# Optimization experiments

Hardware: AMD Instinct MI355X
Metric: run time of the kernel (lower is better)

## Reference

```python
import jax, jax.numpy as jnp
import numpy as np
from jax import lax

NUM_GROUPS = 16
POOL_KS = 2
CLAMP_MIN = 0.0
CLAMP_MAX = 1.0
EPS = 1e-5


def setup_inputs() -> dict:
    key = jax.random.key(0)
    k1, k2, k3, k4, k5 = jax.random.split(key, 5)
    B, Cin, H, W = 32, 64, 128, 128
    Cout, K = 128, 3
    x = jax.random.normal(k1, (B, Cin, H, W), dtype=jnp.float32)
    fan_in = Cin * K * K
    bound = 1.0 / np.sqrt(fan_in)
    conv_w = jax.random.uniform(k2, (Cout, Cin, K, K), jnp.float32, -bound, bound)
    conv_b = jax.random.uniform(k3, (Cout,), jnp.float32, -bound, bound)
    gn_w = jnp.ones((Cout,), jnp.float32)
    gn_b = jnp.zeros((Cout,), jnp.float32)
    scale = jnp.ones((Cout, 1, 1), jnp.float32)
    return {"x": x, "conv_w": conv_w, "conv_b": conv_b,
            "gn_w": gn_w, "gn_b": gn_b, "scale": scale}


def reference(x, conv_w, conv_b, gn_w, gn_b, scale):
    # Conv2d, stride=1, padding=0  -> (B, Cout, Ho, Wo)
    y = lax.conv_general_dilated(
        x, conv_w, window_strides=(1, 1), padding="VALID",
        dimension_numbers=("NCHW", "OIHW", "NCHW"))
    y = y + conv_b[None, :, None, None]
    B, C, H, W = y.shape
    G = NUM_GROUPS
    # GroupNorm (biased variance, as in torch)
    yg = y.reshape(B, G, C // G, H, W)
    mean = jnp.mean(yg, axis=(2, 3, 4), keepdims=True)
    var = jnp.mean(jnp.square(yg), axis=(2, 3, 4), keepdims=True) - jnp.square(mean)
    yn = (yg - mean) * lax.rsqrt(var + EPS)
    yn = yn.reshape(B, C, H, W) * gn_w[None, :, None, None] + gn_b[None, :, None, None]
    # per-channel scale
    yn = yn * scale[None, :, :, :]
    # MaxPool2d(kernel=POOL_KS, stride=POOL_KS), VALID
    pooled = lax.reduce_window(
        yn, -jnp.inf, lax.max,
        window_dimensions=(1, 1, POOL_KS, POOL_KS),
        window_strides=(1, 1, POOL_KS, POOL_KS),
        padding="VALID")
    return jnp.clip(pooled, CLAMP_MIN, CLAMP_MAX)
```

## Files before the change

kernel.cpp:

```cpp
#include <hip/hip_runtime.h>
#include <stdint.h>
#include <stddef.h>

#define HIN 128
#define WIN 128
#define CINC 64
#define COUTC 128
#define HO 126
#define WO 126
#define HP 63
#define WP 63
#define NB 32
#define NG 16

typedef __bf16 bf16x8 __attribute__((ext_vector_type(8)));
typedef float f32x16 __attribute__((ext_vector_type(16)));

#define AS1U(p) ((const __attribute__((address_space(1))) unsigned int*)(p))
#define AS3U(p) ((__attribute__((address_space(3))) unsigned int*)(p))

#define WAITVM_(n) asm volatile("s_waitcnt vmcnt(" #n ")" ::: "memory")
#define WAITVM(n) WAITVM_(n)

__device__ __forceinline__ unsigned int f2bf(float f) {
  unsigned int u = __float_as_uint(f);
  return (u + 0x7fffu + ((u >> 16) & 1u)) >> 16;
}

__global__ __launch_bounds__(256) void wtrans_k(const float* __restrict__ w,
                                                unsigned short* __restrict__ wt2,
                                                float* __restrict__ stats) {
  int i = blockIdx.x * 256 + threadIdx.x;
  if (i < 1024) stats[i] = 0.0f;
  if (i >= 73728) return;
  int j = i & 7;
  int co = (i >> 3) & 127;
  int th = i >> 10;
  int half = th & 1, ks = (th >> 1) & 3, tap = th >> 3;
  int kh = tap / 3, kw = tap - 3 * kh;
  int cin = ks * 16 + half * 8 + j;
  float v = w[((co * CINC + cin) * 3 + kh) * 3 + kw];
  wt2[i] = (unsigned short)f2bf(v);
}

__global__ __launch_bounds__(256, 3) void conv_k(const float* __restrict__ x,
                                                 const unsigned short* __restrict__ wt2,
                                                 const float* __restrict__ conv_b,
                                                 float* __restrict__ out,
                                                 float* __restrict__ stats) {
  __shared__ __align__(16) unsigned int x_lds[10 * 18 * 32];
  __shared__ __align__(16) unsigned int w_lds[4096];

  int t = threadIdx.x;
  int lane = t & 63, wave = t >> 6;
  int wh = wave >> 1, wc = wave & 1;
  int tw = blockIdx.x & 7, th = blockIdx.x >> 3;
  int b = blockIdx.y;
  int oh0 = th * 8, ow0 = tw * 16;
  int half = lane >> 5, m = lane & 31;
  int rot4 = (((int)blockIdx.x + b) % 9) * 4;
  const unsigned int* wg = (const unsigned int*)wt2;
  int wdma_src = wave * 256 + lane * 4;
  int wdma_dst = wave * 256;

#pragma unroll
  for (int j = 0; j < 2; ++j) {
    int rs = j + rot4;
    if (rs >= 36) rs -= 36;
    __builtin_amdgcn_global_load_lds(AS1U(wg + rs * 1024 + wdma_src),
                                     AS3U(&w_lds[j * 1024 + wdma_dst]), 16, 0, 0);
  }

  float bias[2];
#pragma unroll
  for (int nt = 0; nt < 2; ++nt) bias[nt] = conv_b[wc * 64 + nt * 32 + m];

  const float* xb = x + (size_t)b * CINC * HIN * WIN;
#pragma unroll
  for (int k = 0; k < 7; ++k) {
    int i = k * 256 + t;
    if (i < 1600) {
      int c4 = i % 5;
      int j = i / 5;
      int p = j & 31;
      int r = j >> 5;
      int gr = oh0 + r;
      int gc0 = ow0 + c4 * 4;
      float4 v0 = make_float4(0.f, 0.f, 0.f, 0.f);
      float4 v1 = v0;
      if (gr < HIN && gc0 < WIN) {
        const float* base = xb + ((size_t)(2 * p) * HIN + gr) * WIN + gc0;
        v0 = *(const float4*)base;
        v1 = *(const float4*)(base + HIN * WIN);
      }
      float e0[4] = {v0.x, v0.y, v0.z, v0.w};
      float e1[4] = {v1.x, v1.y, v1.z, v1.w};
#pragma unroll
      for (int cc = 0; cc < 4; ++cc) {
        int c = c4 * 4 + cc;
        if (c < 18) {
          unsigned int d = f2bf(e0[cc]) | (f2bf(e1[cc]) << 16);
          x_lds[(r * 18 + c) * 32 + (p ^ ((c & 7) << 2))] = d;
        }
      }
    }
  }
  __syncthreads();

  f32x16 acc[2][2];
#pragma unroll
  for (int nt = 0; nt < 2; ++nt)
#pragma unroll
    for (int mt = 0; mt < 2; ++mt)
#pragma unroll
      for (int r = 0; r < 16; ++r) acc[mt][nt][r] = bias[nt];

  int prb = wh * 4 + (m >> 4);
  int pcc = m & 15;
  int h4 = half * 4;
  int wbl = half * 512 + wc * 256 + m * 4;

#define CONV_KS(ks_, VM, DO_DMA)                                               \
  {                                                                            \
    if (DO_DMA) {                                                              \
      int rs2 = rsb + (ks_) + 2;                                               \
      if (rs2 >= 36) rs2 -= 36;                                                \
      __builtin_amdgcn_global_load_lds(                                        \
          AS1U(wg + rs2 * 1024 + wdma_src),                                    \
          AS3U(&w_lds[(((ks_) + 2) & 3) * 1024 + wdma_dst]), 16, 0, 0);        \
    }                                                                          \
    WAITVM(VM);                                                                \
    __builtin_amdgcn_s_barrier();                                              \
    __builtin_amdgcn_sched_barrier(0);                                         \
    int ax = ((ks_)*8 + h4) ^ swz;                                             \
    bf16x8 afr0 = __builtin_bit_cast(bf16x8, *(const uint4*)&x_lds[ra0 + ax]); \
    bf16x8 afr1 = __builtin_bit_cast(bf16x8, *(const uint4*)&x_lds[ra1 + ax]); \
    int wb = (ks_)*1024 + wbl;                                                 \
    bf16x8 bfr0 = __builtin_bit_cast(bf16x8, *(const uint4*)&w_lds[wb]);       \
    bf16x8 bfr1 = __builtin_bit_cast(bf16x8, *(const uint4*)&w_lds[wb + 128]); \
    __builtin_amdgcn_s_setprio(1);                                             \
    acc[0][0] = __builtin_amdgcn_mfma_f32_32x32x16_bf16(afr0, bfr0, acc[0][0], 0, 0, 0); \
    acc[1][0] = __builtin_amdgcn_mfma_f32_32x32x16_bf16(afr1, bfr0, acc[1][0], 0, 0, 0); \
    acc[0][1] = __builtin_amdgcn_mfma_f32_32x32x16_bf16(afr0, bfr1, acc[0][1], 0, 0, 0); \
    acc[1][1] = __builtin_amdgcn_mfma_f32_32x32x16_bf16(afr1, bfr1, acc[1][1], 0, 0, 0); \
    __builtin_amdgcn_s_setprio(0);                                             \
  }

#pragma unroll 1
  for (int tp = 0; tp < 8; ++tp) {
    int rsb = tp * 4 + rot4;
    if (rsb >= 36) rsb -= 36;
    int tap = rsb >> 2;
    int kh = (tap * 11) >> 5;
    int kw = tap - 3 * kh;
    int c = pcc + kw;
    int swz = (c & 7) << 2;
    int ra0 = (prb + kh) * 576 + c * 32;
    int ra1 = ra0 + 2 * 576;
    CONV_KS(0, 2, 1)
    CONV_KS(1, 2, 1)
    CONV_KS(2, 2, 1)
    CONV_KS(3, 2, 1)
  }
  {
    int rsb = 32 + rot4;
    if (rsb >= 36) rsb -= 36;
    int tap = rsb >> 2;
    int kh = (tap * 11) >> 5;
    int kw = tap - 3 * kh;
    int c = pcc + kw;
    int swz = (c & 7) << 2;
    int ra0 = (prb + kh) * 576 + c * 32;
    int ra1 = ra0 + 2 * 576;
    CONV_KS(0, 2, 1)
    CONV_KS(1, 2, 1)
    CONV_KS(2, 1, 0)
    CONV_KS(3, 0, 0)
  }
#undef CONV_KS

  float s[2] = {0.f, 0.f}, qs[2] = {0.f, 0.f};
#pragma unroll
  for (int nt = 0; nt < 2; ++nt) {
#pragma unroll
    for (int mt = 0; mt < 2; ++mt) {
#pragma unroll
      for (int reg = 0; reg < 16; ++reg) {
        int c16 = (reg & 3) + 4 * half + 8 * ((reg >> 2) & 1);
        int r8 = wh * 4 + mt * 2 + (reg >> 3);
        if ((oh0 + r8) < HO && (ow0 + c16) < WO) {
          float v = acc[mt][nt][reg];
          s[nt] += v;
          qs[nt] += v * v;
        }
      }
    }
  }
#pragma unroll
  for (int nt = 0; nt < 2; ++nt) {
    float sv = s[nt], qv = qs[nt];
    sv += __shfl_xor(sv, 32);
    qv += __shfl_xor(qv, 32);
    sv += __shfl_down(sv, 4, 8);
    qv += __shfl_down(qv, 4, 8);
    sv += __shfl_down(sv, 2, 8);
    qv += __shfl_down(qv, 2, 8);
    sv += __shfl_down(sv, 1, 8);
    qv += __shfl_down(qv, 1, 8);
    if (half == 0 && (m & 7) == 0) {
      int g = wc * 8 + nt * 4 + (m >> 3);
      atomicAdd(&stats[(b * NG + g) * 2 + 0], sv);
      atomicAdd(&stats[(b * NG + g) * 2 + 1], qv);
    }
  }

  __syncthreads();

#pragma unroll
  for (int nt = 0; nt < 2; ++nt) {
    int co = wc * 64 + nt * 32 + m;
#pragma unroll
    for (int mt = 0; mt < 2; ++mt) {
      int oh2l = wh * 2 + mt;
#pragma unroll
      for (int i = 0; i < 4; ++i) {
        int r0 = 2 * i;
        int ow2l = (i & 1) + 2 * half + 4 * (i >> 1);
        float mx = fmaxf(fmaxf(acc[mt][nt][r0], acc[mt][nt][r0 + 1]),
                         fmaxf(acc[mt][nt][r0 + 8], acc[mt][nt][r0 + 9]));
        x_lds[co * 34 + oh2l * 8 + ow2l] = __float_as_uint(mx);
      }
    }
  }
  __syncthreads();

#pragma unroll
  for (int i = 0; i < 2; ++i) {
    int row = t * 2 + i;
    int co = row >> 2, oh2l = row & 3;
    int oh2 = th * 4 + oh2l;
    if (oh2 < HP) {
      const uint2* src = (const uint2*)&x_lds[co * 34 + oh2l * 8];
      uint2 d0 = src[0], d1 = src[1], d2 = src[2], d3 = src[3];
      unsigned int v[8] = {d0.x, d0.y, d1.x, d1.y, d2.x, d2.y, d3.x, d3.y};
      float* ob = out + ((size_t)(b * COUTC + co) * HP + oh2) * WP + tw * 8;
      int n = (tw == 7) ? 7 : 8;
#pragma unroll
      for (int e = 0; e < 8; ++e)
        if (e < n) ob[e] = __uint_as_float(v[e]);
    }
  }
}

__global__ __launch_bounds__(256) void fin_k(float* __restrict__ out,
                                             const float* __restrict__ stats,
                                             const float* __restrict__ gn_w,
                                             const float* __restrict__ gn_b,
                                             const float* __restrict__ scale) {
  const int plane = HP * WP;
  const float inv_cnt = 1.0f / (8.0f * HO * WO);
  int bc = blockIdx.x;
  int c = bc & 127, b = bc >> 7;
  int g = c >> 3;
  float su = stats[(b * NG + g) * 2 + 0];
  float sq = stats[(b * NG + g) * 2 + 1];
  float mean = su * inv_cnt;
  float var = fmaxf(sq * inv_cnt - mean * mean, 0.f);
  float rstd = rsqrtf(var + 1e-5f);
  float gw = gn_w[c], sc = scale[c];
  float A = rstd * gw * sc;
  float Bo = (gn_b[c] - mean * rstd * gw) * sc;

  float* p = out + (size_t)bc * plane;
  int t = threadIdx.x;
  int head = (4 - (bc & 3)) & 3;
  if (t < head) p[t] = fminf(fmaxf(fmaf(p[t], A, Bo), 0.0f), 1.0f);
  int n4 = (plane - head) >> 2;
  float4* p4 = (float4*)(p + head);
  for (int i = t; i < n4; i += 256) {
    float4 v = p4[i];
    v.x = fminf(fmaxf(fmaf(v.x, A, Bo), 0.0f), 1.0f);
    v.y = fminf(fmaxf(fmaf(v.y, A, Bo), 0.0f), 1.0f);
    v.z = fminf(fmaxf(fmaf(v.z, A, Bo), 0.0f), 1.0f);
    v.w = fminf(fmaxf(fmaf(v.w, A, Bo), 0.0f), 1.0f);
    p4[i] = v;
  }
  int done = head + (n4 << 2);
  int tail = plane - done;
  if (t < tail) p[done + t] = fminf(fmaxf(fmaf(p[done + t], A, Bo), 0.0f), 1.0f);
}

extern "C" void kernel_launch(void* const* d_in, const int* in_sizes, int n_in,
                              void* d_out, int out_size, void* d_ws, size_t ws_size,
                              hipStream_t stream) {
  const float* x      = (const float*)d_in[0];
  const float* conv_w = (const float*)d_in[1];
  const float* conv_b = (const float*)d_in[2];
  const float* gn_w   = (const float*)d_in[3];
  const float* gn_b   = (const float*)d_in[4];
  const float* scale  = (const float*)d_in[5];
  float* out = (float*)d_out;

  float* stats        = (float*)d_ws;
  unsigned short* wt2 = (unsigned short*)((char*)d_ws + 4096);

  wtrans_k<<<288, 256, 0, stream>>>(conv_w, wt2, stats);

  conv_k<<<dim3(128, NB), 256, 0, stream>>>(x, wt2, conv_b, out, stats);

  fin_k<<<4096, 256, 0, stream>>>(out, stats, gn_w, gn_b, scale);
}
```

Before: 366.3 us.

## Give each wave a private weight ring buffer and drop per-step block barriers

Each wave now DMAs its own copy of the weight slices it needs into a private 3-slot LDS ring, instead of the four waves cooperatively loading one shared 4-slot buffer. Because no wave reads another wave's DMA output, the s_barrier before every k-step is removed and only a per-wave vmcnt wait remains. The cost is more LDS (weights duplicated across waves, 24 KB vs 16 KB) and twice the global-to-LDS DMA traffic for weights. This may reduce occupancy under the 3-blocks-per-CU launch bound.

Result: slower. 381.3 us (+4.1%).

```diff
diff --git a/kernel.cpp b/kernel.cpp
--- a/kernel.cpp
+++ b/kernel.cpp
@@ -49,7 +49,7 @@
                                                  float* __restrict__ out,
                                                  float* __restrict__ stats) {
   __shared__ __align__(16) unsigned int x_lds[10 * 18 * 32];
-  __shared__ __align__(16) unsigned int w_lds[4096];
+  __shared__ __align__(16) unsigned int w_lds[6144];
 
   int t = threadIdx.x;
   int lane = t & 63, wave = t >> 6;
@@ -60,15 +60,17 @@
   int half = lane >> 5, m = lane & 31;
   int rot4 = (((int)blockIdx.x + b) % 9) * 4;
   const unsigned int* wg = (const unsigned int*)wt2;
-  int wdma_src = wave * 256 + lane * 4;
-  int wdma_dst = wave * 256;
+  int wsrc0 = wc * 256 + lane * 4;
+  int wring = wave * 1536;
 
 #pragma unroll
   for (int j = 0; j < 2; ++j) {
     int rs = j + rot4;
     if (rs >= 36) rs -= 36;
-    __builtin_amdgcn_global_load_lds(AS1U(wg + rs * 1024 + wdma_src),
-                                     AS3U(&w_lds[j * 1024 + wdma_dst]), 16, 0, 0);
+    const unsigned int* s0 = wg + rs * 1024 + wsrc0;
+    __builtin_amdgcn_global_load_lds(AS1U(s0), AS3U(&w_lds[wring + j * 512]), 16, 0, 0);
+    __builtin_amdgcn_global_load_lds(AS1U(s0 + 512),
+                                     AS3U(&w_lds[wring + j * 512 + 256]), 16, 0, 0);
   }
 
   float bias[2];
@@ -118,24 +120,26 @@
   int prb = wh * 4 + (m >> 4);
   int pcc = m & 15;
   int h4 = half * 4;
-  int wbl = half * 512 + wc * 256 + m * 4;
-
-#define CONV_KS(ks_, VM, DO_DMA)                                               \
+  int hm = half * 256 + m * 4;
+
+#define CONV_KS(ks_, VM, DO_DMA, SLOT, DSLOT)                                  \
   {                                                                            \
     if (DO_DMA) {                                                              \
       int rs2 = rsb + (ks_) + 2;                                               \
       if (rs2 >= 36) rs2 -= 36;                                                \
+      const unsigned int* s0 = wg + rs2 * 1024 + wsrc0;                        \
       __builtin_amdgcn_global_load_lds(                                        \
-          AS1U(wg + rs2 * 1024 + wdma_src),                                    \
-          AS3U(&w_lds[(((ks_) + 2) & 3) * 1024 + wdma_dst]), 16, 0, 0);        \
+          AS1U(s0), AS3U(&w_lds[wring + (SLOT_T)(DSLOT)*512]), 16, 0, 0);      \
+      __builtin_amdgcn_global_load_lds(                                        \
+          AS1U(s0 + 512), AS3U(&w_lds[wring + (SLOT_T)(DSLOT)*512 + 256]), 16, \
+          0, 0);                                                               \
     }                                                                          \
     WAITVM(VM);                                                                \
-    __builtin_amdgcn_s_barrier();                                              \
     __builtin_amdgcn_sched_barrier(0);                                         \
     int ax = ((ks_)*8 + h4) ^ swz;                                             \
     bf16x8 afr0 = __builtin_bit_cast(bf16x8, *(const uint4*)&x_lds[ra0 + ax]); \
     bf16x8 afr1 = __builtin_bit_cast(bf16x8, *(const uint4*)&x_lds[ra1 + ax]); \
-    int wb = (ks_)*1024 + wbl;                                                 \
+    int wb = wring + (SLOT_T)(SLOT)*512 + hm;                                  \
     bf16x8 bfr0 = __builtin_bit_cast(bf16x8, *(const uint4*)&w_lds[wb]);       \
     bf16x8 bfr1 = __builtin_bit_cast(bf16x8, *(const uint4*)&w_lds[wb + 128]); \
     __builtin_amdgcn_s_setprio(1);                                             \
@@ -146,6 +150,7 @@
     __builtin_amdgcn_s_setprio(0);                                             \
   }
 
+#define SLOT_T int
 #pragma unroll 1
   for (int tp = 0; tp < 8; ++tp) {
     int rsb = tp * 4 + rot4;
@@ -157,10 +162,13 @@
     int swz = (c & 7) << 2;
     int ra0 = (prb + kh) * 576 + c * 32;
     int ra1 = ra0 + 2 * 576;
-    CONV_KS(0, 2, 1)
-    CONV_KS(1, 2, 1)
-    CONV_KS(2, 2, 1)
-    CONV_KS(3, 2, 1)
+    int sb = tp % 3;
+    int sb1 = (sb == 2) ? 0 : sb + 1;
+    int sb2 = (sb1 == 2) ? 0 : sb1 + 1;
+    CONV_KS(0, 4, 1, sb, sb2)
+    CONV_KS(1, 4, 1, sb1, sb)
+    CONV_KS(2, 4, 1, sb2, sb1)
+    CONV_KS(3, 4, 1, sb, sb2)
   }
   {
     int rsb = 32 + rot4;
@@ -172,12 +180,13 @@
     int swz = (c & 7) << 2;
     int ra0 = (prb + kh) * 576 + c * 32;
     int ra1 = ra0 + 2 * 576;
-    CONV_KS(0, 2, 1)
-    CONV_KS(1, 2, 1)
-    CONV_KS(2, 1, 0)
-    CONV_KS(3, 0, 0)
+    CONV_KS(0, 4, 1, 2, 1)
+    CONV_KS(1, 4, 1, 0, 2)
+    CONV_KS(2, 2, 0, 1, 0)
+    CONV_KS(3, 0, 0, 2, 0)
   }
 #undef CONV_KS
+#undef SLOT_T
 
   float s[2] = {0.f, 0.f}, qs[2] = {0.f, 0.f};
 #pragma unroll
```
